# Optimization experiments

Hardware: AMD Instinct MI355X
Metric: run time of the kernel (lower is better)

Reference implementation:

```python
import jax, jax.numpy as jnp
import numpy as np

H = 8          # n_heads
D_HEAD = 64    # head_dim; scores scaled by sqrt(D_HEAD)


def setup_inputs() -> dict:
    key = jax.random.key(0)
    ks = jax.random.split(key, 9)
    B, S, Dm = 8, 1024, 512
    return {
        "input_Q": jax.random.normal(ks[0], (B, S, Dm), jnp.float32),
        "input_K": jax.random.normal(ks[1], (B, S, Dm), jnp.float32),
        "input_V": jax.random.normal(ks[2], (B, S, Dm), jnp.float32),
        "attn_mask": jax.random.randint(ks[3], (B, S, S), 0, 2).astype(bool),
        "edge_encoding": jax.random.normal(ks[4], (B, S, S), jnp.float32),
        "W_Q": jax.random.normal(ks[5], (Dm, Dm), jnp.float32) / np.sqrt(Dm),
        "W_K": jax.random.normal(ks[6], (Dm, Dm), jnp.float32) / np.sqrt(Dm),
        "W_V": jax.random.normal(ks[7], (Dm, Dm), jnp.float32) / np.sqrt(Dm),
        "W_fc": jax.random.normal(ks[8], (Dm, Dm), jnp.float32) / np.sqrt(Dm),
    }


def reference(input_Q, input_K, input_V, attn_mask, edge_encoding, W_Q, W_K, W_V, W_fc):
    B, S, Dm = input_Q.shape
    # project and split heads: [B, H, S, d_head]
    def heads(x, W):
        return (x @ W).reshape(B, S, H, D_HEAD).transpose(0, 2, 1, 3)
    Q = heads(input_Q, W_Q)
    K = heads(input_K, W_K)
    V = heads(input_V, W_V)
    scores = jnp.einsum("bhqd,bhkd->bhqk", Q, K) / np.sqrt(D_HEAD)
    scores = scores + edge_encoding[:, None, :, :]
    scores = jnp.where(attn_mask[:, None, :, :], jnp.float32(-1e9), scores)
    attn = jax.nn.softmax(scores, axis=-1)
    context = jnp.einsum("bhqk,bhkd->bhqd", attn, V)
    context = context.transpose(0, 2, 1, 3).reshape(B, S, Dm)
    output = context @ W_fc
    scores_avg = scores.sum(axis=1) / H  # [B, S, S]
    return output, scores_avg
```

## Files before the change

### kernel.cpp

```cpp
#include <hip/hip_runtime.h>
#include <math.h>

#define B_ 8
#define S_ 1024
#define DM 512
#define H_ 8
#define DH 64

typedef _Float16 h4 __attribute__((ext_vector_type(4)));
typedef _Float16 h8 __attribute__((ext_vector_type(8)));
typedef float f4 __attribute__((ext_vector_type(4)));

#define MFMA16(a, b, c) __builtin_amdgcn_mfma_f32_16x16x32_f16(a, b, c, 0, 0, 0)

__global__ __launch_bounds__(256) void cast_x(
    const float* __restrict__ x0, const float* __restrict__ x1,
    const float* __restrict__ x2, _Float16* __restrict__ y0,
    _Float16* __restrict__ y1, _Float16* __restrict__ y2) {
  const float* x = (blockIdx.y == 0) ? x0 : (blockIdx.y == 1) ? x1 : x2;
  _Float16* y = (blockIdx.y == 0) ? y0 : (blockIdx.y == 1) ? y1 : y2;
  size_t i = (size_t)blockIdx.x * 1024 + (size_t)threadIdx.x * 4;
  float4 v = *(const float4*)(x + i);
  h4 hv = {(_Float16)v.x, (_Float16)v.y, (_Float16)v.z, (_Float16)v.w};
  *(h4*)(y + i) = hv;
}

__global__ __launch_bounds__(256) void cast_w(
    const float* __restrict__ w0, const float* __restrict__ w1,
    const float* __restrict__ w2, const float* __restrict__ w3,
    _Float16* __restrict__ t0, _Float16* __restrict__ t1,
    _Float16* __restrict__ t2, _Float16* __restrict__ t3) {
  const float* W;
  _Float16* T;
  switch (blockIdx.z) {
    case 0: W = w0; T = t0; break;
    case 1: W = w1; T = t1; break;
    case 2: W = w2; T = t2; break;
    default: W = w3; T = t3; break;
  }
  __shared__ _Float16 ts[64][72];
  const int t = threadIdx.x;
  const int r = t >> 2, c0 = (t & 3) * 16;
  const int n0 = blockIdx.x * 64, k0 = blockIdx.y * 64;
#pragma unroll
  for (int i = 0; i < 4; i++) {
    float4 v = *(const float4*)&W[(size_t)(k0 + r) * 512 + n0 + c0 + i * 4];
    h4 hv = {(_Float16)v.x, (_Float16)v.y, (_Float16)v.z, (_Float16)v.w};
    *(h4*)&ts[r][c0 + i * 4] = hv;
  }
  __syncthreads();
  alignas(16) _Float16 outv[16];
#pragma unroll
  for (int i = 0; i < 16; i++) outv[i] = ts[c0 + i][r];
  *(uint4*)&T[(size_t)(n0 + r) * 512 + k0 + c0] = *(uint4*)&outv[0];
  *(uint4*)&T[(size_t)(n0 + r) * 512 + k0 + c0 + 8] = *(uint4*)&outv[8];
}

__global__ __launch_bounds__(256) void gemm_qkv(
    const _Float16* __restrict__ Xq, const _Float16* __restrict__ Xk,
    const _Float16* __restrict__ Xv, const _Float16* __restrict__ Wt,
    _Float16* __restrict__ Qh, _Float16* __restrict__ Kh,
    _Float16* __restrict__ Vth) {
  const int z = blockIdx.z;
  const int id = blockIdx.x + 4 * blockIdx.y;
  const int c = id & 7, r = id >> 3;
  const int by = c + 8 * (r & 7);
  const int bx = r >> 3;
  const _Float16* A = (z == 0) ? Xq : (z == 1) ? Xk : Xv;
  const _Float16* Bt = Wt + (size_t)z * 512 * 512;
  __shared__ _Float16 Sh[128 * 144];
#define AS(rr, cc) Sh[(rr) * 72 + (cc)]
#define BS(rr, cc) Sh[9216 + (rr) * 72 + (cc)]
  const int t = threadIdx.x, lane = t & 63, w = t >> 6;
  const int quad = lane >> 4, l16 = lane & 15;
  const int row0 = by * 128, col0 = bx * 128;
  const int wm = (w & 1) * 64, wn = (w >> 1) * 64;
  const int gr = t >> 3, gc = (t & 7) * 8;
  f4 acc[4][4] = {};
  uint4 pa[4], pb[4];
#pragma unroll
  for (int i = 0; i < 4; i++) {
    pa[i] = *(const uint4*)&A[(size_t)(row0 + gr + 32 * i) * DM + gc];
    pb[i] = *(const uint4*)&Bt[(size_t)(col0 + gr + 32 * i) * DM + gc];
  }
  for (int k0 = 0; k0 < DM; k0 += 64) {
    __syncthreads();
#pragma unroll
    for (int i = 0; i < 4; i++) {
      *(uint4*)&AS(gr + 32 * i, gc) = pa[i];
      *(uint4*)&BS(gr + 32 * i, gc) = pb[i];
    }
    __syncthreads();
    if (k0 + 64 < DM) {
#pragma unroll
      for (int i = 0; i < 4; i++) {
        pa[i] = *(const uint4*)&A[(size_t)(row0 + gr + 32 * i) * DM + k0 + 64 + gc];
        pb[i] = *(const uint4*)&Bt[(size_t)(col0 + gr + 32 * i) * DM + k0 + 64 + gc];
      }
    }
    h8 af[4][2], bf[4][2];
#pragma unroll
    for (int m = 0; m < 4; m++) {
      af[m][0] = *(h8*)&AS(wm + m * 16 + l16, quad * 8);
      af[m][1] = *(h8*)&AS(wm + m * 16 + l16, 32 + quad * 8);
    }
#pragma unroll
    for (int n = 0; n < 4; n++) {
      bf[n][0] = *(h8*)&BS(wn + n * 16 + l16, quad * 8);
      bf[n][1] = *(h8*)&BS(wn + n * 16 + l16, 32 + quad * 8);
    }
#pragma unroll
    for (int m = 0; m < 4; m++)
#pragma unroll
      for (int n = 0; n < 4; n++) {
        acc[m][n] = MFMA16(af[m][0], bf[n][0], acc[m][n]);
        acc[m][n] = MFMA16(af[m][1], bf[n][1], acc[m][n]);
      }
  }
  __syncthreads();
  if (z < 2) {
    _Float16* C = (z == 0) ? Qh : Kh;
#pragma unroll
    for (int m = 0; m < 4; m++)
#pragma unroll
      for (int n = 0; n < 4; n++)
#pragma unroll
        for (int reg = 0; reg < 4; reg++)
          Sh[(wm + m * 16 + quad * 4 + reg) * 144 + wn + n * 16 + l16] =
              (_Float16)acc[m][n][reg];
    __syncthreads();
    const int rr = t >> 4;
    const int cs = (t & 15) * 8;
#pragma unroll
    for (int i = 0; i < 8; i++) {
      int row = rr + 16 * i;
      *(uint4*)&C[(size_t)(row0 + row) * DM + col0 + cs] =
          *(uint4*)&Sh[row * 144 + cs];
    }
  } else {
#pragma unroll
    for (int m = 0; m < 4; m++)
#pragma unroll
      for (int n = 0; n < 4; n++) {
        h4 vv = {(_Float16)acc[m][n][0], (_Float16)acc[m][n][1],
                 (_Float16)acc[m][n][2], (_Float16)acc[m][n][3]};
        *(h4*)&Sh[(wn + n * 16 + l16) * 144 + wm + m * 16 + quad * 4] = vv;
      }
    __syncthreads();
    const int rr = t >> 4;
    const int cs = (t & 15) * 8;
    const int b = row0 >> 10, s0 = row0 & 1023;
#pragma unroll
    for (int i = 0; i < 8; i++) {
      int cg = col0 + rr + 16 * i;
      int h = cg >> 6, d = cg & 63;
      *(uint4*)&Vth[((size_t)(b * 8 + h) * 64 + d) * S_ + s0 + cs] =
          *(uint4*)&Sh[(rr + 16 * i) * 144 + cs];
    }
  }
#undef AS
#undef BS
}

__global__ __launch_bounds__(256) void gemm_fc(
    const _Float16* __restrict__ A, const _Float16* __restrict__ Bt,
    float* __restrict__ C) {
  const int id = blockIdx.x + 4 * blockIdx.y;
  const int c = id & 7, r = id >> 3;
  const int by = c + 8 * (r & 15);
  const int bx = r >> 4;
  __shared__ _Float16 As[64][72], Bs[128][72];
  const int t = threadIdx.x, lane = t & 63, w = t >> 6;
  const int quad = lane >> 4, l16 = lane & 15;
  const int row0 = by * 64, col0 = bx * 128;
  const int wm = (w & 1) * 32, wn = (w >> 1) * 64;
  const int gr = t >> 3, gc = (t & 7) * 8;
  f4 acc[2][4] = {};
  uint4 pa[2], pb[4];
#pragma unroll
  for (int i = 0; i < 2; i++)
    pa[i] = *(const uint4*)&A[(size_t)(row0 + gr + 32 * i) * DM + gc];
#pragma unroll
  for (int i = 0; i < 4; i++)
    pb[i] = *(const uint4*)&Bt[(size_t)(col0 + gr + 32 * i) * DM + gc];
  for (int k0 = 0; k0 < DM; k0 += 64) {
    __syncthreads();
#pragma unroll
    for (int i = 0; i < 2; i++) *(uint4*)&As[gr + 32 * i][gc] = pa[i];
#pragma unroll
    for (int i = 0; i < 4; i++) *(uint4*)&Bs[gr + 32 * i][gc] = pb[i];
    __syncthreads();
    if (k0 + 64 < DM) {
#pragma unroll
      for (int i = 0; i < 2; i++)
        pa[i] = *(const uint4*)&A[(size_t)(row0 + gr + 32 * i) * DM + k0 + 64 + gc];
#pragma unroll
      for (int i = 0; i < 4; i++)
        pb[i] = *(const uint4*)&Bt[(size_t)(col0 + gr + 32 * i) * DM + k0 + 64 + gc];
    }
    h8 af[2][2], bf[4][2];
#pragma unroll
    for (int m = 0; m < 2; m++) {
      af[m][0] = *(h8*)&As[wm + m * 16 + l16][quad * 8];
      af[m][1] = *(h8*)&As[wm + m * 16 + l16][32 + quad * 8];
    }
#pragma unroll
    for (int n = 0; n < 4; n++) {
      bf[n][0] = *(h8*)&Bs[wn + n * 16 + l16][quad * 8];
      bf[n][1] = *(h8*)&Bs[wn + n * 16 + l16][32 + quad * 8];
    }
#pragma unroll
    for (int m = 0; m < 2; m++)
#pragma unroll
      for (int n = 0; n < 4; n++) {
        acc[m][n] = MFMA16(af[m][0], bf[n][0], acc[m][n]);
        acc[m][n] = MFMA16(af[m][1], bf[n][1], acc[m][n]);
      }
  }
#pragma unroll
  for (int m = 0; m < 2; m++)
#pragma unroll
    for (int n = 0; n < 4; n++)
#pragma unroll
      for (int reg = 0; reg < 4; reg++) {
        size_t row = row0 + wm + m * 16 + quad * 4 + reg;
        size_t col = col0 + wn + n * 16 + l16;
        C[row * DM + col] = acc[m][n][reg];
      }
}

__global__ __launch_bounds__(256) void scores_mfma(
    const _Float16* __restrict__ Qh, const _Float16* __restrict__ Kh,
    const int* __restrict__ mask, const float* __restrict__ edge,
    float* __restrict__ out1, _Float16* __restrict__ Ehs) {
  const int b = blockIdx.z;
  const int id = blockIdx.x + 8 * blockIdx.y;
  const int iy = id & 7, jx = id >> 3;
  const int i0 = iy * 128, j0 = jx * 128;
  const _Float16* A = Qh + (size_t)b * S_ * DM;
  const _Float16* Bt = Kh + (size_t)b * S_ * DM;
  __shared__ _Float16 As[128][72], Bs[128][72];
  const int t = threadIdx.x, lane = t & 63, w = t >> 6;
  const int quad = lane >> 4, l16 = lane & 15;
  const int wm = (w & 1) * 64, wn = (w >> 1) * 64;
  const int gr = t >> 3, gc = (t & 7) * 8;
  f4 acc[4][4] = {};
  uint4 pa[4], pb[4];
#pragma unroll
  for (int i = 0; i < 4; i++) {
    pa[i] = *(const uint4*)&A[(size_t)(i0 + gr + 32 * i) * DM + gc];
    pb[i] = *(const uint4*)&Bt[(size_t)(j0 + gr + 32 * i) * DM + gc];
  }
  for (int k0 = 0; k0 < DM; k0 += 64) {
    __syncthreads();
#pragma unroll
    for (int i = 0; i < 4; i++) {
      *(uint4*)&As[gr + 32 * i][gc] = pa[i];
      *(uint4*)&Bs[gr + 32 * i][gc] = pb[i];
    }
    __syncthreads();
    if (k0 + 64 < DM) {
#pragma unroll
      for (int i = 0; i < 4; i++) {
        pa[i] = *(const uint4*)&A[(size_t)(i0 + gr + 32 * i) * DM + k0 + 64 + gc];
        pb[i] = *(const uint4*)&Bt[(size_t)(j0 + gr + 32 * i) * DM + k0 + 64 + gc];
      }
    }
    h8 af[4][2], bf[4][2];
#pragma unroll
    for (int m = 0; m < 4; m++) {
      af[m][0] = *(h8*)&As[wm + m * 16 + l16][quad * 8];
      af[m][1] = *(h8*)&As[wm + m * 16 + l16][32 + quad * 8];
    }
#pragma unroll
    for (int n = 0; n < 4; n++) {
      bf[n][0] = *(h8*)&Bs[wn + n * 16 + l16][quad * 8];
      bf[n][1] = *(h8*)&Bs[wn + n * 16 + l16][32 + quad * 8];
    }
#pragma unroll
    for (int m = 0; m < 4; m++)
#pragma unroll
      for (int n = 0; n < 4; n++) {
        acc[m][n] = MFMA16(af[m][0], bf[n][0], acc[m][n]);
        acc[m][n] = MFMA16(af[m][1], bf[n][1], acc[m][n]);
      }
  }
  const int jt_base = j0 >> 6;
#pragma unroll
  for (int m = 0; m < 4; m++)
#pragma unroll
    for (int reg = 0; reg < 4; reg++) {
      size_t gi = i0 + wm + m * 16 + quad * 4 + reg;
      size_t rowb = ((size_t)b * S_ + gi) * S_;
      const int jt = jt_base + (wn >> 6);
      size_t ehrow = (((size_t)b * 16 + jt) * 1024 + gi) * 64 + l16 * 4;
      h4 ev;
#pragma unroll
      for (int n = 0; n < 4; n++) {
        size_t idx = rowb + j0 + wn + n * 16 + l16;
        int mk = mask[idx];
        float e = edge[idx];
        out1[idx] = mk ? -1e9f : (acc[m][n][reg] * (1.0f / 64.0f) + e);
        ev[n] = mk ? (_Float16)(-65504.0f) : (_Float16)e;
      }
      *(h4*)&Ehs[ehrow] = ev;
    }
}

__global__ __launch_bounds__(256) void flash_mfma(
    const _Float16* __restrict__ Qh, const _Float16* __restrict__ Kh,
    const _Float16* __restrict__ Vth, const _Float16* __restrict__ Ehs,
    _Float16* __restrict__ ctxh) {
  __shared__ _Float16 Ps[128][72], Ks[64][72], Vt[64][72];
  const int t = threadIdx.x, lane = t & 63, w = t >> 6;
  const int quad = lane >> 4, l16 = lane & 15;
  const int g = blockIdx.x + 8 * blockIdx.y;
  const int c = g & 7, r = g >> 3;
  const int bh = c + 8 * (r & 7);
  const int qb = r >> 3;
  const int b = bh >> 3, h = bh & 7;
  const int q0 = qb * 128;
  const size_t bS = (size_t)b * S_;
  const int sr = t >> 3, sc = (t & 7) * 8;
  const int qw = w * 32;

#pragma unroll
  for (int i = 0; i < 4; i++)
    *(uint4*)&Ps[sr + 32 * i][sc] =
        *(const uint4*)&Qh[(bS + q0 + sr + 32 * i) * DM + h * DH + sc];
  __syncthreads();
  h8 aq[2][2];
#pragma unroll
  for (int m = 0; m < 2; m++)
#pragma unroll
    for (int k = 0; k < 2; k++)
      aq[m][k] = *(h8*)&Ps[qw + m * 16 + l16][k * 32 + quad * 8];

  uint4 kv[4];
  kv[0] = *(const uint4*)&Kh[(bS + sr) * DM + h * DH + sc];
  kv[1] = *(const uint4*)&Kh[(bS + sr + 32) * DM + h * DH + sc];
  kv[2] = *(const uint4*)&Vth[((size_t)bh * 64 + sr) * S_ + sc];
  kv[3] = *(const uint4*)&Vth[((size_t)bh * 64 + sr + 32) * S_ + sc];
  h4 evh[2][4];
#pragma unroll
  for (int m = 0; m < 2; m++)
#pragma unroll
    for (int reg = 0; reg < 4; reg++)
      evh[m][reg] = *(const h4*)&Ehs[(((size_t)b * 16 + 0) * 1024 + q0 + qw +
                                      m * 16 + quad * 4 + reg) *
                                         64 +
                                     l16 * 4];

  f4 acco[2][4] = {};
  float m_run[2][4], l_run[2][4];
#pragma unroll
  for (int m = 0; m < 2; m++)
#pragma unroll
    for (int rr = 0; rr < 4; rr++) {
      m_run[m][rr] = -INFINITY;
      l_run[m][rr] = 0.f;
    }

  for (int kb = 0; kb < S_; kb += 64) {
    __syncthreads();
    *(uint4*)&Ks[sr][sc] = kv[0];
    *(uint4*)&Ks[sr + 32][sc] = kv[1];
    *(uint4*)&Vt[sr][sc] = kv[2];
    *(uint4*)&Vt[sr + 32][sc] = kv[3];
    __syncthreads();
    const int kn = kb + 64;
    h4 evn[2][4];
    if (kn < S_) {
      kv[0] = *(const uint4*)&Kh[(bS + kn + sr) * DM + h * DH + sc];
      kv[1] = *(const uint4*)&Kh[(bS + kn + sr + 32) * DM + h * DH + sc];
      kv[2] = *(const uint4*)&Vth[((size_t)bh * 64 + sr) * S_ + kn + sc];
      kv[3] = *(const uint4*)&Vth[((size_t)bh * 64 + sr + 32) * S_ + kn + sc];
      const size_t ehb = ((size_t)b * 16 + (kn >> 6)) * 1024;
#pragma unroll
      for (int m = 0; m < 2; m++)
#pragma unroll
        for (int reg = 0; reg < 4; reg++)
          evn[m][reg] =
              *(const h4*)&Ehs[(ehb + q0 + qw + m * 16 + quad * 4 + reg) * 64 +
                               l16 * 4];
    }
    f4 accs[2][4] = {};
#pragma unroll
    for (int n = 0; n < 4; n++) {
      h8 b0 = *(h8*)&Ks[n * 16 + l16][quad * 8];
      h8 b1 = *(h8*)&Ks[n * 16 + l16][32 + quad * 8];
#pragma unroll
      for (int m = 0; m < 2; m++) {
        accs[m][n] = MFMA16(aq[m][0], b0, accs[m][n]);
        accs[m][n] = MFMA16(aq[m][1], b1, accs[m][n]);
      }
    }
    float sv[2][4][4];
#pragma unroll
    for (int m = 0; m < 2; m++)
#pragma unroll
      for (int n = 0; n < 4; n++)
#pragma unroll
        for (int reg = 0; reg < 4; reg++)
          sv[m][n][reg] = accs[m][n][reg] * 0.125f + (float)evh[m][reg][n];
#pragma unroll
    for (int m = 0; m < 2; m++)
#pragma unroll
      for (int reg = 0; reg < 4; reg++) {
        float mx = fmaxf(fmaxf(sv[m][0][reg], sv[m][1][reg]),
                         fmaxf(sv[m][2][reg], sv[m][3][reg]));
#pragma unroll
        for (int off = 1; off < 16; off <<= 1)
          mx = fmaxf(mx, __shfl_xor(mx, off, 16));
        float mnew = fmaxf(m_run[m][reg], mx);
        float alpha = __expf(m_run[m][reg] - mnew);
        m_run[m][reg] = mnew;
        float psum = 0.f;
#pragma unroll
        for (int n = 0; n < 4; n++) {
          float p = __expf(sv[m][n][reg] - mnew);
          sv[m][n][reg] = p;
          psum += p;
        }
#pragma unroll
        for (int off = 1; off < 16; off <<= 1)
          psum += __shfl_xor(psum, off, 16);
        l_run[m][reg] = l_run[m][reg] * alpha + psum;
#pragma unroll
        for (int d = 0; d < 4; d++) acco[m][d][reg] *= alpha;
      }
#pragma unroll
    for (int m = 0; m < 2; m++)
#pragma unroll
      for (int n = 0; n < 4; n++)
#pragma unroll
        for (int reg = 0; reg < 4; reg++)
          Ps[qw + m * 16 + quad * 4 + reg][n * 16 + l16] =
              (_Float16)sv[m][n][reg];
    h8 ap[2][2];
#pragma unroll
    for (int m = 0; m < 2; m++)
#pragma unroll
      for (int k = 0; k < 2; k++)
        ap[m][k] = *(h8*)&Ps[qw + m * 16 + l16][k * 32 + quad * 8];
#pragma unroll
    for (int d = 0; d < 4; d++) {
      h8 bv0 = *(h8*)&Vt[d * 16 + l16][quad * 8];
      h8 bv1 = *(h8*)&Vt[d * 16 + l16][32 + quad * 8];
#pragma unroll
      for (int m = 0; m < 2; m++) {
        acco[m][d] = MFMA16(ap[m][0], bv0, acco[m][d]);
        acco[m][d] = MFMA16(ap[m][1], bv1, acco[m][d]);
      }
    }
    if (kn < S_) {
#pragma unroll
      for (int m = 0; m < 2; m++)
#pragma unroll
        for (int reg = 0; reg < 4; reg++) evh[m][reg] = evn[m][reg];
    }
  }
#pragma unroll
  for (int m = 0; m < 2; m++)
#pragma unroll
    for (int d = 0; d < 4; d++)
#pragma unroll
      for (int reg = 0; reg < 4; reg++)
        Ps[qw + m * 16 + quad * 4 + reg][d * 16 + l16] =
            (_Float16)(acco[m][d][reg] / l_run[m][reg]);
  __syncthreads();
  const int orr = t >> 3, ocs = (t & 7) * 8;
#pragma unroll
  for (int i = 0; i < 4; i++) {
    int row = orr + 32 * i;
    *(uint4*)&ctxh[(bS + q0 + row) * DM + h * DH + ocs] =
        *(uint4*)&Ps[row][ocs];
  }
}

extern "C" void kernel_launch(void* const* d_in, const int* in_sizes, int n_in,
                              void* d_out, int out_size, void* d_ws,
                              size_t ws_size, hipStream_t stream) {
  const float* Xq = (const float*)d_in[0];
  const float* Xk = (const float*)d_in[1];
  const float* Xv = (const float*)d_in[2];
  const int* mask = (const int*)d_in[3];
  const float* edge = (const float*)d_in[4];
  const float* Wq = (const float*)d_in[5];
  const float* Wk = (const float*)d_in[6];
  const float* Wv = (const float*)d_in[7];
  const float* Wfc = (const float*)d_in[8];

  float* out0 = (float*)d_out;
  float* out1 = out0 + (size_t)B_ * S_ * DM;

  const size_t NE = (size_t)B_ * S_ * DM;
  char* ws = (char*)d_ws;
  _Float16* Qh = (_Float16*)ws;
  _Float16* Kh = Qh + NE;
  _Float16* Vth = Kh + NE;
  _Float16* Xhq = Vth + NE;
  _Float16* Xhk = Xhq + NE;
  _Float16* Xhv = Xhk + NE;
  _Float16* Wt = Xhv + NE;
  _Float16* Wtf = Wt + 3 * 512 * 512;
  _Float16* Ehs = Wt + 4 * 512 * 512;
  _Float16* ctxh = Xhq;

  dim3 blk(256);
  cast_x<<<dim3(4096, 3), blk, 0, stream>>>(Xq, Xk, Xv, Xhq, Xhk, Xhv);
  cast_w<<<dim3(8, 8, 4), blk, 0, stream>>>(Wq, Wk, Wv, Wfc, Wt,
                                            Wt + 512 * 512, Wt + 2 * 512 * 512,
                                            Wtf);
  gemm_qkv<<<dim3(4, 64, 3), blk, 0, stream>>>(Xhq, Xhk, Xhv, Wt, Qh, Kh, Vth);
  scores_mfma<<<dim3(8, 8, 8), blk, 0, stream>>>(Qh, Kh, mask, edge, out1,
                                                 Ehs);
  flash_mfma<<<dim3(8, 64), blk, 0, stream>>>(Qh, Kh, Vth, Ehs, ctxh);
  gemm_fc<<<dim3(4, 128), blk, 0, stream>>>(ctxh, Wtf, out0);
}
```

Before: 393.3 us.

## Load MFMA operands directly from global memory, dropping LDS staging and prefetch

In all GEMM kernels and the attention kernel, the LDS staging of A/B, K and V tiles, along with the register prefetch double-buffering and block barriers, is removed. Each wave now loads its MFMA fragments straight from global memory and relies on L1/L2 caching for reuse across waves. The edge-encoding prefetch is also replaced with an in-loop load. This removes barriers and LDS traffic, but it also removes latency hiding and raises redundant global/L2 traffic, since several waves re-read the same rows.

```diff
diff --git a/kernel.cpp b/kernel.cpp
--- a/kernel.cpp
+++ b/kernel.cpp
@@ -69,45 +69,23 @@
   const _Float16* A = (z == 0) ? Xq : (z == 1) ? Xk : Xv;
   const _Float16* Bt = Wt + (size_t)z * 512 * 512;
   __shared__ _Float16 Sh[128 * 144];
-#define AS(rr, cc) Sh[(rr) * 72 + (cc)]
-#define BS(rr, cc) Sh[9216 + (rr) * 72 + (cc)]
   const int t = threadIdx.x, lane = t & 63, w = t >> 6;
   const int quad = lane >> 4, l16 = lane & 15;
   const int row0 = by * 128, col0 = bx * 128;
   const int wm = (w & 1) * 64, wn = (w >> 1) * 64;
-  const int gr = t >> 3, gc = (t & 7) * 8;
   f4 acc[4][4] = {};
-  uint4 pa[4], pb[4];
-#pragma unroll
-  for (int i = 0; i < 4; i++) {
-    pa[i] = *(const uint4*)&A[(size_t)(row0 + gr + 32 * i) * DM + gc];
-    pb[i] = *(const uint4*)&Bt[(size_t)(col0 + gr + 32 * i) * DM + gc];
-  }
+  const _Float16* Ab = A + (size_t)(row0 + wm + l16) * DM + quad * 8;
+  const _Float16* Bb = Bt + (size_t)(col0 + wn + l16) * DM + quad * 8;
   for (int k0 = 0; k0 < DM; k0 += 64) {
-    __syncthreads();
-#pragma unroll
-    for (int i = 0; i < 4; i++) {
-      *(uint4*)&AS(gr + 32 * i, gc) = pa[i];
-      *(uint4*)&BS(gr + 32 * i, gc) = pb[i];
-    }
-    __syncthreads();
-    if (k0 + 64 < DM) {
-#pragma unroll
-      for (int i = 0; i < 4; i++) {
-        pa[i] = *(const uint4*)&A[(size_t)(row0 + gr + 32 * i) * DM + k0 + 64 + gc];
-        pb[i] = *(const uint4*)&Bt[(size_t)(col0 + gr + 32 * i) * DM + k0 + 64 + gc];
-      }
-    }
     h8 af[4][2], bf[4][2];
 #pragma unroll
     for (int m = 0; m < 4; m++) {
-      af[m][0] = *(h8*)&AS(wm + m * 16 + l16, quad * 8);
-      af[m][1] = *(h8*)&AS(wm + m * 16 + l16, 32 + quad * 8);
-    }
-#pragma unroll
-    for (int n = 0; n < 4; n++) {
-      bf[n][0] = *(h8*)&BS(wn + n * 16 + l16, quad * 8);
-      bf[n][1] = *(h8*)&BS(wn + n * 16 + l16, 32 + quad * 8);
+      const _Float16* ap = Ab + (size_t)m * 16 * DM + k0;
+      const _Float16* bp = Bb + (size_t)m * 16 * DM + k0;
+      af[m][0] = *(const h8*)ap;
+      af[m][1] = *(const h8*)(ap + 32);
+      bf[m][0] = *(const h8*)bp;
+      bf[m][1] = *(const h8*)(bp + 32);
     }
 #pragma unroll
     for (int m = 0; m < 4; m++)
@@ -117,7 +95,6 @@
         acc[m][n] = MFMA16(af[m][1], bf[n][1], acc[m][n]);
       }
   }
-  __syncthreads();
   if (z < 2) {
     _Float16* C = (z == 0) ? Qh : Kh;
 #pragma unroll
@@ -158,8 +135,6 @@
           *(uint4*)&Sh[(rr + 16 * i) * 144 + cs];
     }
   }
-#undef AS
-#undef BS
 }
 
 __global__ __launch_bounds__(256) void gemm_fc(
@@ -169,45 +144,26 @@
   const int c = id & 7, r = id >> 3;
   const int by = c + 8 * (r & 15);
   const int bx = r >> 4;
-  __shared__ _Float16 As[64][72], Bs[128][72];
   const int t = threadIdx.x, lane = t & 63, w = t >> 6;
   const int quad = lane >> 4, l16 = lane & 15;
   const int row0 = by * 64, col0 = bx * 128;
   const int wm = (w & 1) * 32, wn = (w >> 1) * 64;
-  const int gr = t >> 3, gc = (t & 7) * 8;
   f4 acc[2][4] = {};
-  uint4 pa[2], pb[4];
-#pragma unroll
-  for (int i = 0; i < 2; i++)
-    pa[i] = *(const uint4*)&A[(size_t)(row0 + gr + 32 * i) * DM + gc];
-#pragma unroll
-  for (int i = 0; i < 4; i++)
-    pb[i] = *(const uint4*)&Bt[(size_t)(col0 + gr + 32 * i) * DM + gc];
+  const _Float16* Ab = A + (size_t)(row0 + wm + l16) * DM + quad * 8;
+  const _Float16* Bb = Bt + (size_t)(col0 + wn + l16) * DM + quad * 8;
   for (int k0 = 0; k0 < DM; k0 += 64) {
-    __syncthreads();
-#pragma unroll
-    for (int i = 0; i < 2; i++) *(uint4*)&As[gr + 32 * i][gc] = pa[i];
-#pragma unroll
-    for (int i = 0; i < 4; i++) *(uint4*)&Bs[gr + 32 * i][gc] = pb[i];
-    __syncthreads();
-    if (k0 + 64 < DM) {
-#pragma unroll
-      for (int i = 0; i < 2; i++)
-        pa[i] = *(const uint4*)&A[(size_t)(row0 + gr + 32 * i) * DM + k0 + 64 + gc];
-#pragma unroll
-      for (int i = 0; i < 4; i++)
-        pb[i] = *(const uint4*)&Bt[(size_t)(col0 + gr + 32 * i) * DM + k0 + 64 + gc];
-    }
     h8 af[2][2], bf[4][2];
 #pragma unroll
     for (int m = 0; m < 2; m++) {
-      af[m][0] = *(h8*)&As[wm + m * 16 + l16][quad * 8];
-      af[m][1] = *(h8*)&As[wm + m * 16 + l16][32 + quad * 8];
+      const _Float16* ap = Ab + (size_t)m * 16 * DM + k0;
+      af[m][0] = *(const h8*)ap;
+      af[m][1] = *(const h8*)(ap + 32);
     }
 #pragma unroll
     for (int n = 0; n < 4; n++) {
-      bf[n][0] = *(h8*)&Bs[wn + n * 16 + l16][quad * 8];
-      bf[n][1] = *(h8*)&Bs[wn + n * 16 + l16][32 + quad * 8];
+      const _Float16* bp = Bb + (size_t)n * 16 * DM + k0;
+      bf[n][0] = *(const h8*)bp;
+      bf[n][1] = *(const h8*)(bp + 32);
     }
 #pragma unroll
     for (int m = 0; m < 2; m++)
@@ -239,43 +195,22 @@
   const int i0 = iy * 128, j0 = jx * 128;
   const _Float16* A = Qh + (size_t)b * S_ * DM;
   const _Float16* Bt = Kh + (size_t)b * S_ * DM;
-  __shared__ _Float16 As[128][72], Bs[128][72];
   const int t = threadIdx.x, lane = t & 63, w = t >> 6;
   const int quad = lane >> 4, l16 = lane & 15;
   const int wm = (w & 1) * 64, wn = (w >> 1) * 64;
-  const int gr = t >> 3, gc = (t & 7) * 8;
   f4 acc[4][4] = {};
-  uint4 pa[4], pb[4];
-#pragma unroll
-  for (int i = 0; i < 4; i++) {
-    pa[i] = *(const uint4*)&A[(size_t)(i0 + gr + 32 * i) * DM + gc];
-    pb[i] = *(const uint4*)&Bt[(size_t)(j0 + gr + 32 * i) * DM + gc];
-  }
+  const _Float16* Ab = A + (size_t)(i0 + wm + l16) * DM + quad * 8;
+  const _Float16* Bb = Bt + (size_t)(j0 + wn + l16) * DM + quad * 8;
   for (int k0 = 0; k0 < DM; k0 += 64) {
-    __syncthreads();
-#pragma unroll
-    for (int i = 0; i < 4; i++) {
-      *(uint4*)&As[gr + 32 * i][gc] = pa[i];
-      *(uint4*)&Bs[gr + 32 * i][gc] = pb[i];
-    }
-    __syncthreads();
-    if (k0 + 64 < DM) {
-#pragma unroll
-      for (int i = 0; i < 4; i++) {
-        pa[i] = *(const uint4*)&A[(size_t)(i0 + gr + 32 * i) * DM + k0 + 64 + gc];
-        pb[i] = *(const uint4*)&Bt[(size_t)(j0 + gr + 32 * i) * DM + k0 + 64 + gc];
-      }
-    }
     h8 af[4][2], bf[4][2];
 #pragma unroll
     for (int m = 0; m < 4; m++) {
-      af[m][0] = *(h8*)&As[wm + m * 16 + l16][quad * 8];
-      af[m][1] = *(h8*)&As[wm + m * 16 + l16][32 + quad * 8];
-    }
-#pragma unroll
-    for (int n = 0; n < 4; n++) {
-      bf[n][0] = *(h8*)&Bs[wn + n * 16 + l16][quad * 8];
-      bf[n][1] = *(h8*)&Bs[wn + n * 16 + l16][32 + quad * 8];
+      const _Float16* ap = Ab + (size_t)m * 16 * DM + k0;
+      const _Float16* bp = Bb + (size_t)m * 16 * DM + k0;
+      af[m][0] = *(const h8*)ap;
+      af[m][1] = *(const h8*)(ap + 32);
+      bf[m][0] = *(const h8*)bp;
+      bf[m][1] = *(const h8*)(bp + 32);
     }
 #pragma unroll
     for (int m = 0; m < 4; m++)
@@ -311,7 +246,7 @@
     const _Float16* __restrict__ Qh, const _Float16* __restrict__ Kh,
     const _Float16* __restrict__ Vth, const _Float16* __restrict__ Ehs,
     _Float16* __restrict__ ctxh) {
-  __shared__ _Float16 Ps[128][72], Ks[64][72], Vt[64][72];
+  __shared__ _Float16 Ps[128][72];
   const int t = threadIdx.x, lane = t & 63, w = t >> 6;
   const int quad = lane >> 4, l16 = lane & 15;
   const int g = blockIdx.x + 8 * blockIdx.y;
@@ -321,35 +256,15 @@
   const int b = bh >> 3, h = bh & 7;
   const int q0 = qb * 128;
   const size_t bS = (size_t)b * S_;
-  const int sr = t >> 3, sc = (t & 7) * 8;
   const int qw = w * 32;
 
-#pragma unroll
-  for (int i = 0; i < 4; i++)
-    *(uint4*)&Ps[sr + 32 * i][sc] =
-        *(const uint4*)&Qh[(bS + q0 + sr + 32 * i) * DM + h * DH + sc];
-  __syncthreads();
   h8 aq[2][2];
 #pragma unroll
   for (int m = 0; m < 2; m++)
 #pragma unroll
     for (int k = 0; k < 2; k++)
-      aq[m][k] = *(h8*)&Ps[qw + m * 16 + l16][k * 32 + quad * 8];
-
-  uint4 kv[4];
-  kv[0] = *(const uint4*)&Kh[(bS + sr) * DM + h * DH + sc];
-  kv[1] = *(const uint4*)&Kh[(bS + sr + 32) * DM + h * DH + sc];
-  kv[2] = *(const uint4*)&Vth[((size_t)bh * 64 + sr) * S_ + sc];
-  kv[3] = *(const uint4*)&Vth[((size_t)bh * 64 + sr + 32) * S_ + sc];
-  h4 evh[2][4];
-#pragma unroll
-  for (int m = 0; m < 2; m++)
-#pragma unroll
-    for (int reg = 0; reg < 4; reg++)
-      evh[m][reg] = *(const h4*)&Ehs[(((size_t)b * 16 + 0) * 1024 + q0 + qw +
-                                      m * 16 + quad * 4 + reg) *
-                                         64 +
-                                     l16 * 4];
+      aq[m][k] = *(const h8*)&Qh[(bS + q0 + qw + m * 16 + l16) * DM + h * DH +
+                                 k * 32 + quad * 8];
 
   f4 acco[2][4] = {};
   float m_run[2][4], l_run[2][4];
@@ -361,34 +276,25 @@
       l_run[m][rr] = 0.f;
     }
 
+  const _Float16* Kb = Kh + bS * DM + h * DH + quad * 8;
+  const _Float16* Vb = Vth + (size_t)bh * 64 * S_ + quad * 8;
+
   for (int kb = 0; kb < S_; kb += 64) {
-    __syncthreads();
-    *(uint4*)&Ks[sr][sc] = kv[0];
-    *(uint4*)&Ks[sr + 32][sc] = kv[1];
-    *(uint4*)&Vt[sr][sc] = kv[2];
-    *(uint4*)&Vt[sr + 32][sc] = kv[3];
-    __syncthreads();
-    const int kn = kb + 64;
-    h4 evn[2][4];
-    if (kn < S_) {
-      kv[0] = *(const uint4*)&Kh[(bS + kn + sr) * DM + h * DH + sc];
-      kv[1] = *(const uint4*)&Kh[(bS + kn + sr + 32) * DM + h * DH + sc];
-      kv[2] = *(const uint4*)&Vth[((size_t)bh * 64 + sr) * S_ + kn + sc];
-      kv[3] = *(const uint4*)&Vth[((size_t)bh * 64 + sr + 32) * S_ + kn + sc];
-      const size_t ehb = ((size_t)b * 16 + (kn >> 6)) * 1024;
-#pragma unroll
-      for (int m = 0; m < 2; m++)
-#pragma unroll
-        for (int reg = 0; reg < 4; reg++)
-          evn[m][reg] =
-              *(const h4*)&Ehs[(ehb + q0 + qw + m * 16 + quad * 4 + reg) * 64 +
-                               l16 * 4];
-    }
+    const size_t ehb = ((size_t)b * 16 + (kb >> 6)) * 1024;
+    h4 evh[2][4];
+#pragma unroll
+    for (int m = 0; m < 2; m++)
+#pragma unroll
+      for (int reg = 0; reg < 4; reg++)
+        evh[m][reg] =
+            *(const h4*)&Ehs[(ehb + q0 + qw + m * 16 + quad * 4 + reg) * 64 +
+                             l16 * 4];
     f4 accs[2][4] = {};
 #pragma unroll
     for (int n = 0; n < 4; n++) {
-      h8 b0 = *(h8*)&Ks[n * 16 + l16][quad * 8];
-      h8 b1 = *(h8*)&Ks[n * 16 + l16][32 + quad * 8];
+      const _Float16* kp = Kb + (size_t)(kb + n * 16 + l16) * DM;
+      h8 b0 = *(const h8*)kp;
+      h8 b1 = *(const h8*)(kp + 32);
 #pragma unroll
       for (int m = 0; m < 2; m++) {
         accs[m][n] = MFMA16(aq[m][0], b0, accs[m][n]);
@@ -445,19 +351,14 @@
         ap[m][k] = *(h8*)&Ps[qw + m * 16 + l16][k * 32 + quad * 8];
 #pragma unroll
     for (int d = 0; d < 4; d++) {
-      h8 bv0 = *(h8*)&Vt[d * 16 + l16][quad * 8];
-      h8 bv1 = *(h8*)&Vt[d * 16 + l16][32 + quad * 8];
+      const _Float16* vp = Vb + (size_t)(d * 16 + l16) * S_ + kb;
+      h8 bv0 = *(const h8*)vp;
+      h8 bv1 = *(const h8*)(vp + 32);
 #pragma unroll
       for (int m = 0; m < 2; m++) {
         acco[m][d] = MFMA16(ap[m][0], bv0, acco[m][d]);
         acco[m][d] = MFMA16(ap[m][1], bv1, acco[m][d]);
       }
-    }
-    if (kn < S_) {
-#pragma unroll
-      for (int m = 0; m < 2; m++)
-#pragma unroll
-        for (int reg = 0; reg < 4; reg++) evh[m][reg] = evn[m][reg];
     }
   }
 #pragma unroll
```

Measured after the change: 408.2 us. 3.8% more time.
